# Kernel optimization log

Hardware: AMD Instinct MI355X
Metric: run time of the kernel (lower is better)

Reference implementation:

```python
import jax, jax.numpy as jnp
import numpy as np

C = 256
CQK = C // 8  # 32

def setup_inputs() -> dict:
    key = jax.random.key(0)
    ks = jax.random.split(key, 8)
    x = jax.random.normal(ks[0], (4, C, 64, 64), dtype=jnp.float32)
    Wq = jax.random.normal(ks[1], (CQK, C), dtype=jnp.float32) * 0.02
    bq = jnp.zeros((CQK,), dtype=jnp.float32)
    Wk = jax.random.normal(ks[2], (CQK, C), dtype=jnp.float32) * 0.02
    bk = jnp.zeros((CQK,), dtype=jnp.float32)
    Wv = jax.random.normal(ks[3], (C, C), dtype=jnp.float32) * 0.02
    bv = jnp.zeros((C,), dtype=jnp.float32)
    # torch init: gamma = zeros(1); use small nonzero so backward path through attention is exercised? -> stay faithful: zeros
    gamma = jnp.zeros((1,), dtype=jnp.float32)
    return {"x": x, "Wq": Wq, "bq": bq, "Wk": Wk, "bk": bk, "Wv": Wv, "bv": bv, "gamma": gamma}


def reference(x, Wq, bq, Wk, bk, Wv, bv, gamma):
    B, Cc, H, W = x.shape
    N = H * W
    xf = x.reshape(B, Cc, N)                              # B,C,N
    # 1x1 convs == per-position matmuls
    q = jnp.einsum('bcn,dc->bnd', xf, Wq) + bq            # B,N,C/8  (proj_query permuted)
    k = jnp.einsum('bcn,dc->bdn', xf, Wk) + bk[:, None]   # B,C/8,N
    v = jnp.einsum('bcn,dc->bdn', xf, Wv) + bv[:, None]   # B,C,N
    energy = jnp.einsum('bnd,bdm->bnm', q, k)             # B,N,N
    attention = jax.nn.softmax(energy, axis=-1)           # softmax over last dim
    # out[b,c,m] = sum_n v[b,c,n] * attention[b,m,n]
    out = jnp.einsum('bcn,bmn->bcm', v, attention)
    out = out.reshape(B, Cc, H, W)
    return gamma * out + x
```

## Files before the change

kernel.cpp:

```cpp
#include <hip/hip_runtime.h>

#define B_  4
#define N_  4096
#define C_  256
#define D_  32

typedef __attribute__((ext_vector_type(8))) short bf8;
typedef __attribute__((ext_vector_type(4))) float f4;

__device__ __forceinline__ unsigned short bft(float f) {
    unsigned u = __builtin_bit_cast(unsigned, f);
    return (unsigned short)((u + 0x8000u) >> 16);
}
__device__ __forceinline__ unsigned pk2(float a, float b) {
    unsigned ua = __builtin_bit_cast(unsigned, a) + 0x8000u;
    unsigned ub = __builtin_bit_cast(unsigned, b) + 0x8000u;
    return __builtin_amdgcn_perm(ub, ua, 0x07060302u);
}

__global__ __launch_bounds__(256) void prep(
    const float* __restrict__ Wq, const float* __restrict__ Wk,
    const float* __restrict__ Wv,
    unsigned short* __restrict__ Wqkb, unsigned short* __restrict__ Wvb)
{
    int i = blockIdx.x * 256 + threadIdx.x;
    if (i < 8192)       Wqkb[i] = bft(Wq[i]);
    else if (i < 16384) Wqkb[i] = bft(Wk[i - 8192]);
    Wvb[i] = bft(Wv[i]);
}

__global__ __launch_bounds__(256) void qkv(
    const float* __restrict__ x,
    const unsigned short* __restrict__ Wqkb, const unsigned short* __restrict__ Wvb,
    const float* __restrict__ bq, const float* __restrict__ bk,
    const float* __restrict__ bv,
    unsigned short* __restrict__ qb, unsigned short* __restrict__ kb,
    unsigned short* __restrict__ vb)
{
    const int b = blockIdx.y, n0 = blockIdx.x * 32;
    const int t = threadIdx.x;
    const int lane = t & 63, w = t >> 6, c15 = lane & 15, g = lane >> 4;

    __shared__ __align__(16) unsigned short xs[32][264];

    {
        const int r = t >> 3, cg = t & 7;
        #pragma unroll
        for (int it = 0; it < 8; ++it) {
            int c = r + 32 * it;
            float4 v = *(const float4*)(x + ((size_t)(b * C_ + c)) * N_ + n0 + cg * 4);
            xs[cg * 4 + 0][c] = bft(v.x);
            xs[cg * 4 + 1][c] = bft(v.y);
            xs[cg * 4 + 2][c] = bft(v.z);
            xs[cg * 4 + 3][c] = bft(v.w);
        }
    }
    __syncthreads();

    f4 qkacc[2]; f4 vacc[2][4];
    const f4 fz = {0.f, 0.f, 0.f, 0.f};
    qkacc[0] = fz; qkacc[1] = fz;
    #pragma unroll
    for (int nt = 0; nt < 2; ++nt)
        #pragma unroll
        for (int ct = 0; ct < 4; ++ct) vacc[nt][ct] = fz;

    const unsigned short* wqk = Wqkb + (w * 16 + c15) * C_ + g * 8;
    const unsigned short* wv0 = Wvb + (w * 64 + c15) * C_ + g * 8;
    const unsigned short* xsp = &xs[c15][g * 8];

    #pragma unroll
    for (int ks = 0; ks < 8; ++ks) {
        bf8 xf0 = *(const bf8*)(xsp + ks * 32);
        bf8 xf1 = *(const bf8*)(xsp + 16 * 264 + ks * 32);
        bf8 af  = *(const bf8*)(wqk + ks * 32);
        qkacc[0] = __builtin_amdgcn_mfma_f32_16x16x32_bf16(af, xf0, qkacc[0], 0, 0, 0);
        qkacc[1] = __builtin_amdgcn_mfma_f32_16x16x32_bf16(af, xf1, qkacc[1], 0, 0, 0);
        #pragma unroll
        for (int ct = 0; ct < 4; ++ct) {
            bf8 bfv = *(const bf8*)(wv0 + ct * 16 * C_ + ks * 32);
            vacc[0][ct] = __builtin_amdgcn_mfma_f32_16x16x32_bf16(xf0, bfv, vacc[0][ct], 0, 0, 0);
            vacc[1][ct] = __builtin_amdgcn_mfma_f32_16x16x32_bf16(xf1, bfv, vacc[1][ct], 0, 0, 0);
        }
    }

    {
        float4 bias = (w < 2) ? *(const float4*)(bq + (w & 1) * 16 + 4 * g)
                              : *(const float4*)(bk + (w & 1) * 16 + 4 * g);
        float sc = (w < 2) ? 1.44269504f : 1.0f;
        unsigned short* base = (w < 2) ? qb : kb;
        int d0 = (w & 1) * 16 + 4 * g;
        #pragma unroll
        for (int nt = 0; nt < 2; ++nt) {
            int n = n0 + nt * 16 + c15;
            f4 a = qkacc[nt];
            uint2 pk;
            pk.x = pk2((a.x + bias.x) * sc, (a.y + bias.y) * sc);
            pk.y = pk2((a.z + bias.z) * sc, (a.w + bias.w) * sc);
            *(uint2*)(base + ((size_t)(b * N_ + n)) * D_ + d0) = pk;
        }
    }
    #pragma unroll
    for (int ct = 0; ct < 4; ++ct) {
        int cout = w * 64 + ct * 16 + c15;
        float bvv = bv[cout];
        #pragma unroll
        for (int nt = 0; nt < 2; ++nt) {
            f4 a = vacc[nt][ct];
            uint2 pk;
            pk.x = pk2(a.x + bvv, a.y + bvv);
            pk.y = pk2(a.z + bvv, a.w + bvv);
            *(uint2*)(vb + ((size_t)(b * C_ + cout)) * (size_t)N_ + n0 + nt * 16 + 4 * g) = pk;
        }
    }
}

__global__ __launch_bounds__(512, 2) void attn(
    const unsigned short* __restrict__ qb, const unsigned short* __restrict__ kb,
    const unsigned short* __restrict__ vb, const float* __restrict__ x,
    const float* __restrict__ gamma, float* __restrict__ out)
{
    const int b = blockIdx.z, c0 = blockIdx.y * 128, m0 = blockIdx.x * 128;
    const int t = threadIdx.x;
    const int lane = t & 63, w = t >> 6, c15 = lane & 15, g = lane >> 4;
    const int pm = w & 3, ph = w >> 2;
    const int mtg = w & 1, ctg = (w >> 1) & 1, ksh = w >> 2;

    __shared__ __align__(16) unsigned short Ps[2][128][136];
    __shared__ float l_s[2][128];

    const f4 fz = {0.f, 0.f, 0.f, 0.f};

    bf8 qf[2];
    #pragma unroll
    for (int mi = 0; mi < 2; ++mi)
        qf[mi] = *(const bf8*)(qb + ((size_t)(b * N_ + m0 + (2 * pm + mi) * 16 + c15)) * D_ + g * 8);

    bf8 kf[4];
    #pragma unroll
    for (int ff = 0; ff < 4; ++ff)
        kf[ff] = *(const bf8*)(kb + ((size_t)(b * N_ + (ph * 4 + ff) * 16 + c15)) * D_ + g * 8);

    f4 acc[4][4];
    #pragma unroll
    for (int mt = 0; mt < 4; ++mt)
        #pragma unroll
        for (int ct = 0; ct < 4; ++ct) acc[mt][ct] = fz;
    float lrun[2] = {0.f, 0.f};

    const unsigned short* vbase = vb + ((size_t)(b * C_ + c0 + ctg * 64)) * (size_t)N_;

    for (int j0 = 0; j0 < N_; j0 += 128) {
        const int buf = (j0 >> 7) & 1;
        bf8 vf[2][4];
        #pragma unroll
        for (int ki = 0; ki < 2; ++ki)
            #pragma unroll
            for (int ct = 0; ct < 4; ++ct)
                vf[ki][ct] = *(const bf8*)(vbase + (size_t)(ct * 16 + c15) * N_
                                           + j0 + (ksh * 2 + ki) * 32 + g * 8);
        f4 s[2][4];
        #pragma unroll
        for (int mi = 0; mi < 2; ++mi)
            #pragma unroll
            for (int ff = 0; ff < 4; ++ff)
                s[mi][ff] = __builtin_amdgcn_mfma_f32_16x16x32_bf16(kf[ff], qf[mi], fz, 0, 0, 0);
        if (j0 + 128 < N_) {
            #pragma unroll
            for (int ff = 0; ff < 4; ++ff)
                kf[ff] = *(const bf8*)(kb + ((size_t)(b * N_ + j0 + 128 + (ph * 4 + ff) * 16 + c15)) * D_ + g * 8);
        }
        #pragma unroll
        for (int mi = 0; mi < 2; ++mi) {
            #pragma unroll
            for (int ff = 0; ff < 4; ++ff) {
                float p0 = __builtin_amdgcn_exp2f(s[mi][ff].x);
                float p1 = __builtin_amdgcn_exp2f(s[mi][ff].y);
                float p2 = __builtin_amdgcn_exp2f(s[mi][ff].z);
                float p3 = __builtin_amdgcn_exp2f(s[mi][ff].w);
                lrun[mi] += (p0 + p1) + (p2 + p3);
                uint2 pk; pk.x = pk2(p0, p1); pk.y = pk2(p2, p3);
                *(uint2*)&Ps[buf][(2 * pm + mi) * 16 + c15][(ph * 4 + ff) * 16 + 4 * g] = pk;
            }
        }
        asm volatile("s_waitcnt lgkmcnt(0)\n\ts_barrier" ::: "memory");
        #pragma unroll
        for (int ki = 0; ki < 2; ++ki) {
            const int kcol = (ksh * 2 + ki) * 32 + g * 8;
            bf8 pf[4];
            #pragma unroll
            for (int mt = 0; mt < 4; ++mt)
                pf[mt] = *(const bf8*)&Ps[buf][(mtg * 4 + mt) * 16 + c15][kcol];
            #pragma unroll
            for (int mt = 0; mt < 4; ++mt)
                #pragma unroll
                for (int ct = 0; ct < 4; ++ct)
                    acc[mt][ct] = __builtin_amdgcn_mfma_f32_16x16x32_bf16(pf[mt], vf[ki][ct], acc[mt][ct], 0, 0, 0);
        }
    }

    #pragma unroll
    for (int mi = 0; mi < 2; ++mi) {
        lrun[mi] += __shfl_xor(lrun[mi], 16);
        lrun[mi] += __shfl_xor(lrun[mi], 32);
    }
    if (lane < 16) {
        l_s[ph][(2 * pm) * 16 + lane]     = lrun[0];
        l_s[ph][(2 * pm + 1) * 16 + lane] = lrun[1];
    }
    __syncthreads();

    float* accs = (float*)&Ps[0][0][0];
    const int pos = w & 3;
    if (ksh == 1) {
        #pragma unroll
        for (int mt = 0; mt < 4; ++mt)
            #pragma unroll
            for (int ct = 0; ct < 4; ++ct)
                *(f4*)&accs[(((pos * 16 + mt * 4 + ct) * 64) + lane) * 4] = acc[mt][ct];
    }
    __syncthreads();
    if (ksh == 0) {
        const float g0 = gamma[0];
        #pragma unroll
        for (int mt = 0; mt < 4; ++mt) {
            const int mrow = (mtg * 4 + mt) * 16;
            float4 la = *(const float4*)&l_s[0][mrow + 4 * g];
            float4 lb = *(const float4*)&l_s[1][mrow + 4 * g];
            float i0 = 1.f / (la.x + lb.x), i1 = 1.f / (la.y + lb.y);
            float i2 = 1.f / (la.z + lb.z), i3 = 1.f / (la.w + lb.w);
            #pragma unroll
            for (int ct = 0; ct < 4; ++ct) {
                f4 o = *(const f4*)&accs[(((pos * 16 + mt * 4 + ct) * 64) + lane) * 4];
                f4 a = acc[mt][ct];
                int c = c0 + (ctg * 4 + ct) * 16 + c15;
                size_t base = ((size_t)(b * C_ + c)) * (size_t)N_ + m0 + mrow + 4 * g;
                float4 xv = *(const float4*)(x + base);
                float4 r;
                r.x = g0 * ((a.x + o.x) * i0) + xv.x;
                r.y = g0 * ((a.y + o.y) * i1) + xv.y;
                r.z = g0 * ((a.z + o.z) * i2) + xv.z;
                r.w = g0 * ((a.w + o.w) * i3) + xv.w;
                *(float4*)(out + base) = r;
            }
        }
    }
}

extern "C" void kernel_launch(void* const* d_in, const int* in_sizes, int n_in,
                              void* d_out, int out_size, void* d_ws, size_t ws_size,
                              hipStream_t stream) {
    const float* x     = (const float*)d_in[0];
    const float* Wq    = (const float*)d_in[1];
    const float* bq    = (const float*)d_in[2];
    const float* Wk    = (const float*)d_in[3];
    const float* bk    = (const float*)d_in[4];
    const float* Wv    = (const float*)d_in[5];
    const float* bv    = (const float*)d_in[6];
    const float* gamma = (const float*)d_in[7];
    float* out = (float*)d_out;

    unsigned short* qb   = (unsigned short*)d_ws;
    unsigned short* kb   = qb + (size_t)B_ * N_ * D_;
    unsigned short* vb   = kb + (size_t)B_ * N_ * D_;
    unsigned short* Wqkb = vb + (size_t)B_ * C_ * N_;
    unsigned short* Wvb  = Wqkb + 64 * C_;

    prep<<<256, 256, 0, stream>>>(Wq, Wk, Wv, Wqkb, Wvb);
    qkv<<<dim3(128, 4), 256, 0, stream>>>(x, Wqkb, Wvb, bq, bk, bv, qb, kb, vb);
    attn<<<dim3(32, 2, 4), 512, 0, stream>>>(qb, kb, vb, x, gamma, out);
}
```

Before: 172.7 us.

## Shrink attention tile to 64 query rows with swizzled LDS and more blocks

Each attention block now handles 64 query positions instead of 128. Each of the 8 waves computes one 16-key slice of scores for all 64 queries, and the wave-to-channel split changes accordingly. The P tile in shared memory uses an XOR swizzle instead of padding, the block index is remapped to a 1D grid that interleaves batch and channel halves, and launch bounds target 4 blocks per CU. The aim is more blocks for occupancy, fewer bank conflicts and lower register pressure. The cost is twice as many blocks each re-reading K and V, so V traffic per output doubles.

Result: faster. 167.2 us (-3.2%).

```diff
diff --git a/kernel.cpp b/kernel.cpp
--- a/kernel.cpp
+++ b/kernel.cpp
@@ -115,126 +115,121 @@
     }
 }
 
-__global__ __launch_bounds__(512, 2) void attn(
+__global__ __launch_bounds__(512, 4) void attn(
     const unsigned short* __restrict__ qb, const unsigned short* __restrict__ kb,
     const unsigned short* __restrict__ vb, const float* __restrict__ x,
     const float* __restrict__ gamma, float* __restrict__ out)
 {
-    const int b = blockIdx.z, c0 = blockIdx.y * 128, m0 = blockIdx.x * 128;
+    const int bid = blockIdx.x;
+    const int combo = bid & 7, mb = bid >> 3;
+    const int b = combo >> 1, c0 = (combo & 1) * 128, m0 = mb * 64;
     const int t = threadIdx.x;
     const int lane = t & 63, w = t >> 6, c15 = lane & 15, g = lane >> 4;
-    const int pm = w & 3, ph = w >> 2;
-    const int mtg = w & 1, ctg = (w >> 1) & 1, ksh = w >> 2;
-
-    __shared__ __align__(16) unsigned short Ps[2][128][136];
-    __shared__ float l_s[2][128];
+    const int cq = w & 3, ksh = w >> 2;
+    const int sw = (c15 & 7) << 4;
+
+    __shared__ __align__(16) unsigned short Ps[2][64 * 128];
+    __shared__ float l_s[8][64];
+    __shared__ __align__(16) float l_tot[64];
 
     const f4 fz = {0.f, 0.f, 0.f, 0.f};
 
-    bf8 qf[2];
-    #pragma unroll
-    for (int mi = 0; mi < 2; ++mi)
-        qf[mi] = *(const bf8*)(qb + ((size_t)(b * N_ + m0 + (2 * pm + mi) * 16 + c15)) * D_ + g * 8);
-
-    bf8 kf[4];
-    #pragma unroll
-    for (int ff = 0; ff < 4; ++ff)
-        kf[ff] = *(const bf8*)(kb + ((size_t)(b * N_ + (ph * 4 + ff) * 16 + c15)) * D_ + g * 8);
-
-    f4 acc[4][4];
+    bf8 qf[4];
+    #pragma unroll
+    for (int mi = 0; mi < 4; ++mi)
+        qf[mi] = *(const bf8*)(qb + ((size_t)(b * N_ + m0 + mi * 16 + c15)) * D_ + g * 8);
+
+    bf8 kf = *(const bf8*)(kb + ((size_t)(b * N_ + w * 16 + c15)) * D_ + g * 8);
+
+    f4 acc[4][2];
     #pragma unroll
     for (int mt = 0; mt < 4; ++mt)
         #pragma unroll
-        for (int ct = 0; ct < 4; ++ct) acc[mt][ct] = fz;
-    float lrun[2] = {0.f, 0.f};
-
-    const unsigned short* vbase = vb + ((size_t)(b * C_ + c0 + ctg * 64)) * (size_t)N_;
+        for (int ct = 0; ct < 2; ++ct) acc[mt][ct] = fz;
+    float lrun[4] = {0.f, 0.f, 0.f, 0.f};
+
+    const unsigned short* vbase = vb + ((size_t)(b * C_ + c0 + cq * 32)) * (size_t)N_;
 
     for (int j0 = 0; j0 < N_; j0 += 128) {
         const int buf = (j0 >> 7) & 1;
-        bf8 vf[2][4];
+        char* pbase = (char*)Ps[buf];
+        bf8 vf[2][2];
         #pragma unroll
         for (int ki = 0; ki < 2; ++ki)
             #pragma unroll
-            for (int ct = 0; ct < 4; ++ct)
+            for (int ct = 0; ct < 2; ++ct)
                 vf[ki][ct] = *(const bf8*)(vbase + (size_t)(ct * 16 + c15) * N_
-                                           + j0 + (ksh * 2 + ki) * 32 + g * 8);
-        f4 s[2][4];
-        #pragma unroll
-        for (int mi = 0; mi < 2; ++mi)
-            #pragma unroll
-            for (int ff = 0; ff < 4; ++ff)
-                s[mi][ff] = __builtin_amdgcn_mfma_f32_16x16x32_bf16(kf[ff], qf[mi], fz, 0, 0, 0);
-        if (j0 + 128 < N_) {
-            #pragma unroll
-            for (int ff = 0; ff < 4; ++ff)
-                kf[ff] = *(const bf8*)(kb + ((size_t)(b * N_ + j0 + 128 + (ph * 4 + ff) * 16 + c15)) * D_ + g * 8);
-        }
-        #pragma unroll
-        for (int mi = 0; mi < 2; ++mi) {
-            #pragma unroll
-            for (int ff = 0; ff < 4; ++ff) {
-                float p0 = __builtin_amdgcn_exp2f(s[mi][ff].x);
-                float p1 = __builtin_amdgcn_exp2f(s[mi][ff].y);
-                float p2 = __builtin_amdgcn_exp2f(s[mi][ff].z);
-                float p3 = __builtin_amdgcn_exp2f(s[mi][ff].w);
-                lrun[mi] += (p0 + p1) + (p2 + p3);
-                uint2 pk; pk.x = pk2(p0, p1); pk.y = pk2(p2, p3);
-                *(uint2*)&Ps[buf][(2 * pm + mi) * 16 + c15][(ph * 4 + ff) * 16 + 4 * g] = pk;
-            }
+                                           + j0 + ksh * 64 + ki * 32 + g * 8);
+        f4 s[4];
+        #pragma unroll
+        for (int mi = 0; mi < 4; ++mi)
+            s[mi] = __builtin_amdgcn_mfma_f32_16x16x32_bf16(kf, qf[mi], fz, 0, 0, 0);
+        if (j0 + 128 < N_)
+            kf = *(const bf8*)(kb + ((size_t)(b * N_ + j0 + 128 + w * 16 + c15)) * D_ + g * 8);
+        #pragma unroll
+        for (int mi = 0; mi < 4; ++mi) {
+            float p0 = __builtin_amdgcn_exp2f(s[mi].x);
+            float p1 = __builtin_amdgcn_exp2f(s[mi].y);
+            float p2 = __builtin_amdgcn_exp2f(s[mi].z);
+            float p3 = __builtin_amdgcn_exp2f(s[mi].w);
+            lrun[mi] += (p0 + p1) + (p2 + p3);
+            uint2 pk; pk.x = pk2(p0, p1); pk.y = pk2(p2, p3);
+            *(uint2*)(pbase + (mi * 16 + c15) * 256 + ((w * 32 + 8 * g) ^ sw)) = pk;
         }
         asm volatile("s_waitcnt lgkmcnt(0)\n\ts_barrier" ::: "memory");
         #pragma unroll
         for (int ki = 0; ki < 2; ++ki) {
-            const int kcol = (ksh * 2 + ki) * 32 + g * 8;
+            const int kbyte = (ksh * 128 + ki * 64 + 16 * g) ^ sw;
             bf8 pf[4];
             #pragma unroll
             for (int mt = 0; mt < 4; ++mt)
-                pf[mt] = *(const bf8*)&Ps[buf][(mtg * 4 + mt) * 16 + c15][kcol];
+                pf[mt] = *(const bf8*)(pbase + (mt * 16 + c15) * 256 + kbyte);
             #pragma unroll
             for (int mt = 0; mt < 4; ++mt)
                 #pragma unroll
-                for (int ct = 0; ct < 4; ++ct)
+                for (int ct = 0; ct < 2; ++ct)
                     acc[mt][ct] = __builtin_amdgcn_mfma_f32_16x16x32_bf16(pf[mt], vf[ki][ct], acc[mt][ct], 0, 0, 0);
         }
     }
 
     #pragma unroll
-    for (int mi = 0; mi < 2; ++mi) {
+    for (int mi = 0; mi < 4; ++mi) {
         lrun[mi] += __shfl_xor(lrun[mi], 16);
         lrun[mi] += __shfl_xor(lrun[mi], 32);
     }
     if (lane < 16) {
-        l_s[ph][(2 * pm) * 16 + lane]     = lrun[0];
-        l_s[ph][(2 * pm + 1) * 16 + lane] = lrun[1];
+        #pragma unroll
+        for (int mi = 0; mi < 4; ++mi) l_s[w][mi * 16 + lane] = lrun[mi];
     }
     __syncthreads();
 
-    float* accs = (float*)&Ps[0][0][0];
-    const int pos = w & 3;
+    float* accs = (float*)Ps;
     if (ksh == 1) {
         #pragma unroll
         for (int mt = 0; mt < 4; ++mt)
             #pragma unroll
-            for (int ct = 0; ct < 4; ++ct)
-                *(f4*)&accs[(((pos * 16 + mt * 4 + ct) * 64) + lane) * 4] = acc[mt][ct];
+            for (int ct = 0; ct < 2; ++ct)
+                *(f4*)&accs[(((cq * 8 + mt * 2 + ct) * 64) + lane) * 4] = acc[mt][ct];
+    }
+    if (w == 0) {
+        float sacc = 0.f;
+        #pragma unroll
+        for (int ww = 0; ww < 8; ++ww) sacc += l_s[ww][lane];
+        l_tot[lane] = sacc;
     }
     __syncthreads();
     if (ksh == 0) {
         const float g0 = gamma[0];
         #pragma unroll
         for (int mt = 0; mt < 4; ++mt) {
-            const int mrow = (mtg * 4 + mt) * 16;
-            float4 la = *(const float4*)&l_s[0][mrow + 4 * g];
-            float4 lb = *(const float4*)&l_s[1][mrow + 4 * g];
-            float i0 = 1.f / (la.x + lb.x), i1 = 1.f / (la.y + lb.y);
-            float i2 = 1.f / (la.z + lb.z), i3 = 1.f / (la.w + lb.w);
-            #pragma unroll
-            for (int ct = 0; ct < 4; ++ct) {
-                f4 o = *(const f4*)&accs[(((pos * 16 + mt * 4 + ct) * 64) + lane) * 4];
+            float4 lv = *(const float4*)&l_tot[mt * 16 + 4 * g];
+            float i0 = 1.f / lv.x, i1 = 1.f / lv.y, i2 = 1.f / lv.z, i3 = 1.f / lv.w;
+            #pragma unroll
+            for (int ct = 0; ct < 2; ++ct) {
+                f4 o = *(const f4*)&accs[(((cq * 8 + mt * 2 + ct) * 64) + lane) * 4];
                 f4 a = acc[mt][ct];
-                int c = c0 + (ctg * 4 + ct) * 16 + c15;
-                size_t base = ((size_t)(b * C_ + c)) * (size_t)N_ + m0 + mrow + 4 * g;
+                int c = c0 + cq * 32 + ct * 16 + c15;
+                size_t base = ((size_t)(b * C_ + c)) * (size_t)N_ + m0 + mt * 16 + 4 * g;
                 float4 xv = *(const float4*)(x + base);
                 float4 r;
                 r.x = g0 * ((a.x + o.x) * i0) + xv.x;
@@ -268,5 +263,5 @@
 
     prep<<<256, 256, 0, stream>>>(Wq, Wk, Wv, Wqkb, Wvb);
     qkv<<<dim3(128, 4), 256, 0, stream>>>(x, Wqkb, Wvb, bq, bk, bv, qb, kb, vb);
-    attn<<<dim3(32, 2, 4), 512, 0, stream>>>(qb, kb, vb, x, gamma, out);
-}
+    attn<<<dim3(512), 512, 0, stream>>>(qb, kb, vb, x, gamma, out);
+}
```

## Retile attention to 32-query blocks covering all channels with swizzled P tile

Applied to the files above, without the earlier changes.

The attention kernel now gives each 256-thread block 32 query positions and all 256 channels, instead of 128 queries by 128 channels split across 512 threads. Because every block covers all channels, the QK^T scores and exponentials are computed once per query rather than once per channel half, and the cross-wave accumulator reduction through shared memory goes away. The P tile is stored with an XOR swizzle to avoid LDS bank conflicts, and the launch becomes a flat grid of 512 blocks. In exchange, each block streams the full V matrix for only 32 queries, so V reuse per block falls and global/L2 traffic for V rises.

Result: slower. 220.8 us (+27.8%).

```diff
diff --git a/kernel.cpp b/kernel.cpp
--- a/kernel.cpp
+++ b/kernel.cpp
@@ -115,84 +115,78 @@
     }
 }
 
-__global__ __launch_bounds__(512, 2) void attn(
+__global__ __launch_bounds__(256, 2) void attn(
     const unsigned short* __restrict__ qb, const unsigned short* __restrict__ kb,
     const unsigned short* __restrict__ vb, const float* __restrict__ x,
     const float* __restrict__ gamma, float* __restrict__ out)
 {
-    const int b = blockIdx.z, c0 = blockIdx.y * 128, m0 = blockIdx.x * 128;
+    const int bid = blockIdx.x;
+    const int b = bid & 3, m0 = (bid >> 2) * 32;
     const int t = threadIdx.x;
     const int lane = t & 63, w = t >> 6, c15 = lane & 15, g = lane >> 4;
-    const int pm = w & 3, ph = w >> 2;
-    const int mtg = w & 1, ctg = (w >> 1) & 1, ksh = w >> 2;
-
-    __shared__ __align__(16) unsigned short Ps[2][128][136];
-    __shared__ float l_s[2][128];
+    const int sw = (c15 & 7) << 4;
+
+    __shared__ __align__(16) unsigned short Ps[2][32 * 128];
+    __shared__ float l_s[4][32];
 
     const f4 fz = {0.f, 0.f, 0.f, 0.f};
 
     bf8 qf[2];
     #pragma unroll
-    for (int mi = 0; mi < 2; ++mi)
-        qf[mi] = *(const bf8*)(qb + ((size_t)(b * N_ + m0 + (2 * pm + mi) * 16 + c15)) * D_ + g * 8);
-
-    bf8 kf[4];
-    #pragma unroll
-    for (int ff = 0; ff < 4; ++ff)
-        kf[ff] = *(const bf8*)(kb + ((size_t)(b * N_ + (ph * 4 + ff) * 16 + c15)) * D_ + g * 8);
-
-    f4 acc[4][4];
-    #pragma unroll
-    for (int mt = 0; mt < 4; ++mt)
+    for (int mt = 0; mt < 2; ++mt)
+        qf[mt] = *(const bf8*)(qb + ((size_t)(b * N_ + m0 + mt * 16 + c15)) * D_ + g * 8);
+
+    bf8 kfc[2], kfn[2];
+    #pragma unroll
+    for (int nf = 0; nf < 2; ++nf)
+        kfc[nf] = *(const bf8*)(kb + ((size_t)(b * N_ + w * 32 + nf * 16 + c15)) * D_ + g * 8);
+
+    f4 acc[2][4];
+    #pragma unroll
+    for (int mt = 0; mt < 2; ++mt)
         #pragma unroll
         for (int ct = 0; ct < 4; ++ct) acc[mt][ct] = fz;
-    float lrun[2] = {0.f, 0.f};
-
-    const unsigned short* vbase = vb + ((size_t)(b * C_ + c0 + ctg * 64)) * (size_t)N_;
+    float lr[2] = {0.f, 0.f};
+
+    const unsigned short* vB = vb + ((size_t)(b * C_ + w * 64)) * (size_t)N_;
 
     for (int j0 = 0; j0 < N_; j0 += 128) {
-        const int buf = (j0 >> 7) & 1;
-        bf8 vf[2][4];
-        #pragma unroll
-        for (int ki = 0; ki < 2; ++ki)
+        char* pb = (char*)Ps[(j0 >> 7) & 1];
+        bf8 vf[4][4];
+        #pragma unroll
+        for (int ki = 0; ki < 4; ++ki)
             #pragma unroll
             for (int ct = 0; ct < 4; ++ct)
-                vf[ki][ct] = *(const bf8*)(vbase + (size_t)(ct * 16 + c15) * N_
-                                           + j0 + (ksh * 2 + ki) * 32 + g * 8);
-        f4 s[2][4];
-        #pragma unroll
-        for (int mi = 0; mi < 2; ++mi)
-            #pragma unroll
-            for (int ff = 0; ff < 4; ++ff)
-                s[mi][ff] = __builtin_amdgcn_mfma_f32_16x16x32_bf16(kf[ff], qf[mi], fz, 0, 0, 0);
+                vf[ki][ct] = *(const bf8*)(vB + (size_t)(ct * 16 + c15) * N_
+                                           + j0 + ki * 32 + g * 8);
         if (j0 + 128 < N_) {
             #pragma unroll
-            for (int ff = 0; ff < 4; ++ff)
-                kf[ff] = *(const bf8*)(kb + ((size_t)(b * N_ + j0 + 128 + (ph * 4 + ff) * 16 + c15)) * D_ + g * 8);
-        }
-        #pragma unroll
-        for (int mi = 0; mi < 2; ++mi) {
-            #pragma unroll
-            for (int ff = 0; ff < 4; ++ff) {
-                float p0 = __builtin_amdgcn_exp2f(s[mi][ff].x);
-                float p1 = __builtin_amdgcn_exp2f(s[mi][ff].y);
-                float p2 = __builtin_amdgcn_exp2f(s[mi][ff].z);
-                float p3 = __builtin_amdgcn_exp2f(s[mi][ff].w);
-                lrun[mi] += (p0 + p1) + (p2 + p3);
+            for (int nf = 0; nf < 2; ++nf)
+                kfn[nf] = *(const bf8*)(kb + ((size_t)(b * N_ + j0 + 128 + w * 32 + nf * 16 + c15)) * D_ + g * 8);
+        }
+        #pragma unroll
+        for (int mt = 0; mt < 2; ++mt)
+            #pragma unroll
+            for (int nf = 0; nf < 2; ++nf) {
+                f4 s = __builtin_amdgcn_mfma_f32_16x16x32_bf16(kfc[nf], qf[mt], fz, 0, 0, 0);
+                float p0 = __builtin_amdgcn_exp2f(s.x);
+                float p1 = __builtin_amdgcn_exp2f(s.y);
+                float p2 = __builtin_amdgcn_exp2f(s.z);
+                float p3 = __builtin_amdgcn_exp2f(s.w);
+                lr[mt] += (p0 + p1) + (p2 + p3);
                 uint2 pk; pk.x = pk2(p0, p1); pk.y = pk2(p2, p3);
-                *(uint2*)&Ps[buf][(2 * pm + mi) * 16 + c15][(ph * 4 + ff) * 16 + 4 * g] = pk;
+                *(uint2*)(pb + (mt * 16 + c15) * 256 + ((w * 64 + nf * 32 + 8 * g) ^ sw)) = pk;
             }
-        }
+        kfc[0] = kfn[0]; kfc[1] = kfn[1];
         asm volatile("s_waitcnt lgkmcnt(0)\n\ts_barrier" ::: "memory");
         #pragma unroll
-        for (int ki = 0; ki < 2; ++ki) {
-            const int kcol = (ksh * 2 + ki) * 32 + g * 8;
-            bf8 pf[4];
-            #pragma unroll
-            for (int mt = 0; mt < 4; ++mt)
-                pf[mt] = *(const bf8*)&Ps[buf][(mtg * 4 + mt) * 16 + c15][kcol];
-            #pragma unroll
-            for (int mt = 0; mt < 4; ++mt)
+        for (int ki = 0; ki < 4; ++ki) {
+            bf8 pf[2];
+            #pragma unroll
+            for (int mt = 0; mt < 2; ++mt)
+                pf[mt] = *(const bf8*)(pb + (mt * 16 + c15) * 256 + ((ki * 64 + 16 * g) ^ sw));
+            #pragma unroll
+            for (int mt = 0; mt < 2; ++mt)
                 #pragma unroll
                 for (int ct = 0; ct < 4; ++ct)
                     acc[mt][ct] = __builtin_amdgcn_mfma_f32_16x16x32_bf16(pf[mt], vf[ki][ct], acc[mt][ct], 0, 0, 0);
@@ -200,49 +194,36 @@
     }
 
     #pragma unroll
-    for (int mi = 0; mi < 2; ++mi) {
-        lrun[mi] += __shfl_xor(lrun[mi], 16);
-        lrun[mi] += __shfl_xor(lrun[mi], 32);
-    }
-    if (lane < 16) {
-        l_s[ph][(2 * pm) * 16 + lane]     = lrun[0];
-        l_s[ph][(2 * pm + 1) * 16 + lane] = lrun[1];
-    }
+    for (int mt = 0; mt < 2; ++mt) {
+        lr[mt] += __shfl_xor(lr[mt], 16);
+        lr[mt] += __shfl_xor(lr[mt], 32);
+    }
+    if (lane < 16) { l_s[w][lane] = lr[0]; l_s[w][16 + lane] = lr[1]; }
     __syncthreads();
 
-    float* accs = (float*)&Ps[0][0][0];
-    const int pos = w & 3;
-    if (ksh == 1) {
-        #pragma unroll
-        for (int mt = 0; mt < 4; ++mt)
-            #pragma unroll
-            for (int ct = 0; ct < 4; ++ct)
-                *(f4*)&accs[(((pos * 16 + mt * 4 + ct) * 64) + lane) * 4] = acc[mt][ct];
-    }
-    __syncthreads();
-    if (ksh == 0) {
-        const float g0 = gamma[0];
-        #pragma unroll
-        for (int mt = 0; mt < 4; ++mt) {
-            const int mrow = (mtg * 4 + mt) * 16;
-            float4 la = *(const float4*)&l_s[0][mrow + 4 * g];
-            float4 lb = *(const float4*)&l_s[1][mrow + 4 * g];
-            float i0 = 1.f / (la.x + lb.x), i1 = 1.f / (la.y + lb.y);
-            float i2 = 1.f / (la.z + lb.z), i3 = 1.f / (la.w + lb.w);
-            #pragma unroll
-            for (int ct = 0; ct < 4; ++ct) {
-                f4 o = *(const f4*)&accs[(((pos * 16 + mt * 4 + ct) * 64) + lane) * 4];
-                f4 a = acc[mt][ct];
-                int c = c0 + (ctg * 4 + ct) * 16 + c15;
-                size_t base = ((size_t)(b * C_ + c)) * (size_t)N_ + m0 + mrow + 4 * g;
-                float4 xv = *(const float4*)(x + base);
-                float4 r;
-                r.x = g0 * ((a.x + o.x) * i0) + xv.x;
-                r.y = g0 * ((a.y + o.y) * i1) + xv.y;
-                r.z = g0 * ((a.z + o.z) * i2) + xv.z;
-                r.w = g0 * ((a.w + o.w) * i3) + xv.w;
-                *(float4*)(out + base) = r;
-            }
+    const float g0 = gamma[0];
+    #pragma unroll
+    for (int mt = 0; mt < 2; ++mt) {
+        float4 a0 = *(const float4*)&l_s[0][mt * 16 + 4 * g];
+        float4 a1 = *(const float4*)&l_s[1][mt * 16 + 4 * g];
+        float4 a2 = *(const float4*)&l_s[2][mt * 16 + 4 * g];
+        float4 a3 = *(const float4*)&l_s[3][mt * 16 + 4 * g];
+        float i0 = 1.f / (a0.x + a1.x + a2.x + a3.x);
+        float i1 = 1.f / (a0.y + a1.y + a2.y + a3.y);
+        float i2 = 1.f / (a0.z + a1.z + a2.z + a3.z);
+        float i3 = 1.f / (a0.w + a1.w + a2.w + a3.w);
+        #pragma unroll
+        for (int ct = 0; ct < 4; ++ct) {
+            f4 a = acc[mt][ct];
+            int c = w * 64 + ct * 16 + c15;
+            size_t base = ((size_t)(b * C_ + c)) * (size_t)N_ + m0 + mt * 16 + 4 * g;
+            float4 xv = *(const float4*)(x + base);
+            float4 r;
+            r.x = g0 * (a.x * i0) + xv.x;
+            r.y = g0 * (a.y * i1) + xv.y;
+            r.z = g0 * (a.z * i2) + xv.z;
+            r.w = g0 * (a.w * i3) + xv.w;
+            *(float4*)(out + base) = r;
         }
     }
 }
@@ -268,5 +249,5 @@
 
     prep<<<256, 256, 0, stream>>>(Wq, Wk, Wv, Wqkb, Wvb);
     qkv<<<dim3(128, 4), 256, 0, stream>>>(x, Wqkb, Wvb, bq, bk, bv, qb, kb, vb);
-    attn<<<dim3(32, 2, 4), 512, 0, stream>>>(qb, kb, vb, x, gamma, out);
-}
+    attn<<<dim3(512), 256, 0, stream>>>(qb, kb, vb, x, gamma, out);
+}
```
